# Kernel optimization log

Measured on AMD Instinct MI355X. Metric: run time of the kernel, lower is better.

The kernel has to match this reference:

```python
import jax, jax.numpy as jnp
import numpy as np

B, N, C = 4, 2048, 1024
H = 16
HD = C // H
SCALE = HD ** -0.5


def setup_inputs() -> dict:
    key = jax.random.key(0)
    ks = jax.random.split(key, 5)
    s = 0.02
    return {
        "x": jax.random.normal(ks[0], (B, N, C), dtype=jnp.float32),
        "w_qkv": jax.random.normal(ks[1], (C, 3 * C), dtype=jnp.float32) * s,
        "b_qkv": jnp.zeros((3 * C,), dtype=jnp.float32),
        "w_proj": jax.random.normal(ks[2], (C, C), dtype=jnp.float32) * s,
        "b_proj": jnp.zeros((C,), dtype=jnp.float32),
    }


def reference(x, w_qkv, b_qkv, w_proj, b_proj):
    b, n, c = x.shape
    qkv = x @ w_qkv + b_qkv                       # [b, n, 3c]
    qkv = qkv.reshape(b, n, 3, H, HD)
    qkv = jnp.transpose(qkv, (2, 0, 3, 1, 4))     # [3, b, h, n, hd]
    q, k, v = qkv[0], qkv[1], qkv[2]
    attn = jnp.einsum("bhqd,bhkd->bhqk", q, k) * SCALE
    attn = jax.nn.softmax(attn, axis=-1)
    out = jnp.einsum("bhqk,bhkd->bhqd", attn, v)  # [b, h, n, hd]
    out = jnp.transpose(out, (0, 2, 1, 3)).reshape(b, n, c)
    return out @ w_proj + b_proj
```

## Files before the change

### kernel.cpp

```cpp
#include <hip/hip_runtime.h>
#include <cstdint>
#include <cstddef>


typedef __attribute__((ext_vector_type(8))) short short8;
typedef __attribute__((ext_vector_type(4))) float f32x4;
typedef _Float16 half4 __attribute__((ext_vector_type(4)));

#if __has_builtin(__builtin_amdgcn_exp2f)
#define EXP2F(x) __builtin_amdgcn_exp2f(x)
#else
#define EXP2F(x) __expf((x) * 0.69314718056f)
#endif

__device__ __forceinline__ short f2bf(float x) {
  unsigned u = __builtin_bit_cast(unsigned, x);
  u += 0x7fffu + ((u >> 16) & 1u);
  return (short)(u >> 16);
}

__device__ __forceinline__ unsigned pkh(float a, float b) {
  auto h = __builtin_amdgcn_cvt_pkrtz(a, b);
  return __builtin_bit_cast(unsigned, h);
}

__device__ __forceinline__ void async16(const void* g, void* l) {
  __builtin_amdgcn_global_load_lds(
      (const __attribute__((address_space(1))) unsigned*)g,
      (__attribute__((address_space(3))) unsigned*)l, 16, 0, 0);
}


__global__ __launch_bounds__(256) void convert_kernel(const float* __restrict__ in,
                                                      short* __restrict__ out) {
  int i = blockIdx.x * 256 + threadIdx.x;
  const float4* p = (const float4*)in + (size_t)i * 2;
  float4 a = p[0], b = p[1];
  short8 r;
  r[0] = f2bf(a.x); r[1] = f2bf(a.y); r[2] = f2bf(a.z); r[3] = f2bf(a.w);
  r[4] = f2bf(b.x); r[5] = f2bf(b.y); r[6] = f2bf(b.z); r[7] = f2bf(b.w);
  *((short8*)out + i) = r;
}

__global__ __launch_bounds__(256) void wtrans_kernel(const float* __restrict__ in,
                                                     short* __restrict__ out,
                                                     int K, int N) {
  __shared__ float tile[32][33];
  int n0 = blockIdx.x * 32, k0 = blockIdx.y * 32;
  int tx = threadIdx.x, ty = threadIdx.y;
  for (int r = ty; r < 32; r += 8)
    tile[r][tx] = in[(size_t)(k0 + r) * N + n0 + tx];
  __syncthreads();
  for (int r = ty; r < 32; r += 8)
    out[(size_t)(n0 + r) * K + k0 + tx] = f2bf(tile[tx][r]);
}


template <int MODE>
__global__ __launch_bounds__(512, 2) void gemm_kernel(
    const short* __restrict__ A, const short* __restrict__ Bt,
    const float* __restrict__ bias, int Nn,
    short* __restrict__ qb, short* __restrict__ kb, short* __restrict__ vtb,
    float* __restrict__ outp) {
  constexpr int K = 1024;
  constexpr int NT = K / 64;
  __shared__ __align__(16) short As[3][256 * 64];
  __shared__ __align__(16) short Bs[3][128 * 64];
  const int tid = threadIdx.x, wave = tid >> 6, lane = tid & 63;
  const int quad = lane >> 4, l16 = lane & 15;

  const unsigned bid = blockIdx.x + gridDim.x * blockIdx.y;
  const unsigned c = bid & 7u, j = bid >> 3;
  const unsigned MC = gridDim.y >> 3;
  const unsigned chunk = MC * 8u;
  const unsigned nc = j / chunk, rem = j - nc * chunk;
  const unsigned m_idx = c * MC + (rem >> 3);
  const unsigned n_idx = nc * 8u + (rem & 7u);
  const int m0 = (int)m_idx * 256, n0 = (int)n_idx * 128;

  const int wrow = (wave >> 1) * 64, wcol = (wave & 1) * 64;

  const int srow = tid >> 3;
  const int schunk = ((tid & 7) ^ (srow & 7)) * 8;
  const short* Ag = A + (size_t)(m0 + srow) * K + schunk;
  const short* Bg = Bt + (size_t)(n0 + srow) * K + schunk;
  const int fsw = l16 & 7;

  f32x4 acc[4][4] = {};
  short8 af[4][2], bf[2][2];

  auto stageA = [&](int b, int kt) {
#pragma unroll
    for (int i = 0; i < 4; ++i)
      async16(Ag + (size_t)(i * 64) * K + kt * 64,
              (char*)As[b] + i * 8192 + tid * 16);
  };
  auto stageB = [&](int b, int kt) {
#pragma unroll
    for (int i = 0; i < 2; ++i)
      async16(Bg + (size_t)(i * 64) * K + kt * 64,
              (char*)Bs[b] + i * 8192 + tid * 16);
  };

  stageA(0, 0); stageB(0, 0);
  stageA(1, 1); stageB(1, 1);
  asm volatile("s_waitcnt vmcnt(6)" ::: "memory");
  __builtin_amdgcn_s_barrier();

  int cb = 0;
  for (int t = 0; t < NT; ++t) {
    int sb = cb + 2; if (sb >= 3) sb -= 3;
    const short* Ab = As[cb];
    const short* Bb = Bs[cb];

#pragma unroll
    for (int mf = 0; mf < 4; ++mf)
#pragma unroll
      for (int ks = 0; ks < 2; ++ks)
        af[mf][ks] = *(const short8*)
            &Ab[(wrow + mf * 16 + l16) * 64 + (((ks * 4 + quad) ^ fsw) << 3)];
#pragma unroll
    for (int j2 = 0; j2 < 2; ++j2)
#pragma unroll
      for (int ks = 0; ks < 2; ++ks)
        bf[j2][ks] = *(const short8*)
            &Bb[(wcol + j2 * 16 + l16) * 64 + (((ks * 4 + quad) ^ fsw) << 3)];
    if (t + 2 < NT) stageA(sb, t + 2);
    __builtin_amdgcn_s_barrier();
    __builtin_amdgcn_s_setprio(1);
#pragma unroll
    for (int ks = 0; ks < 2; ++ks)
#pragma unroll
      for (int mf = 0; mf < 4; ++mf)
#pragma unroll
        for (int j2 = 0; j2 < 2; ++j2)
          acc[mf][j2] = __builtin_amdgcn_mfma_f32_16x16x32_bf16(
              af[mf][ks], bf[j2][ks], acc[mf][j2], 0, 0, 0);
    __builtin_amdgcn_s_setprio(0);
    __builtin_amdgcn_s_barrier();

#pragma unroll
    for (int j2 = 0; j2 < 2; ++j2)
#pragma unroll
      for (int ks = 0; ks < 2; ++ks)
        bf[j2][ks] = *(const short8*)
            &Bb[(wcol + (2 + j2) * 16 + l16) * 64 + (((ks * 4 + quad) ^ fsw) << 3)];
    if (t + 2 < NT) stageB(sb, t + 2);
    __builtin_amdgcn_s_barrier();
    __builtin_amdgcn_s_setprio(1);
#pragma unroll
    for (int ks = 0; ks < 2; ++ks)
#pragma unroll
      for (int mf = 0; mf < 4; ++mf)
#pragma unroll
        for (int j2 = 0; j2 < 2; ++j2)
          acc[mf][2 + j2] = __builtin_amdgcn_mfma_f32_16x16x32_bf16(
              af[mf][ks], bf[j2][ks], acc[mf][2 + j2], 0, 0, 0);
    __builtin_amdgcn_s_setprio(0);
    if (t < NT - 2)
      asm volatile("s_waitcnt vmcnt(6)" ::: "memory");
    else if (t == NT - 2)
      asm volatile("s_waitcnt vmcnt(0)" ::: "memory");
    __builtin_amdgcn_s_barrier();
    cb = cb + 1; if (cb >= 3) cb -= 3;
  }

  if (MODE == 0) {
#pragma unroll
    for (int mf = 0; mf < 4; ++mf) {
      int row0 = m0 + wrow + mf * 16 + quad * 4;
      int b = row0 >> 11, n = row0 & 2047;
#pragma unroll
      for (int nf = 0; nf < 4; ++nf) {
        int col = n0 + wcol + nf * 16 + l16;
        float bv = bias[col];
        float v0 = acc[mf][nf][0] + bv, v1 = acc[mf][nf][1] + bv;
        float v2 = acc[mf][nf][2] + bv, v3 = acc[mf][nf][3] + bv;
        int which = col >> 10;
        int h = (col >> 6) & 15;
        int d = col & 63;
        size_t bh = (size_t)(b * 16 + h);
        if (which == 0) {
          const float qs = 0.18033688f;
          size_t base = (bh * 2048 + n) * 64 + d;
          qb[base]       = f2bf(v0 * qs);
          qb[base + 64]  = f2bf(v1 * qs);
          qb[base + 128] = f2bf(v2 * qs);
          qb[base + 192] = f2bf(v3 * qs);
        } else if (which == 1) {
          size_t base = (bh * 2048 + n) * 64 + d;
          kb[base]       = f2bf(v0);
          kb[base + 64]  = f2bf(v1);
          kb[base + 128] = f2bf(v2);
          kb[base + 192] = f2bf(v3);
        } else {
          uint2 pk;
          pk.x = pkh(v0, v1);
          pk.y = pkh(v2, v3);
          *(uint2*)&vtb[(bh * 64 + d) * 2048 + n] = pk;
        }
      }
    }
  } else {
#pragma unroll
    for (int mf = 0; mf < 4; ++mf) {
      int row0 = m0 + wrow + mf * 16 + quad * 4;
#pragma unroll
      for (int nf = 0; nf < 4; ++nf) {
        int col = n0 + wcol + nf * 16 + l16;
        float bv = bias[col];
        outp[(size_t)row0 * Nn + col]       = acc[mf][nf][0] + bv;
        outp[(size_t)(row0 + 1) * Nn + col] = acc[mf][nf][1] + bv;
        outp[(size_t)(row0 + 2) * Nn + col] = acc[mf][nf][2] + bv;
        outp[(size_t)(row0 + 3) * Nn + col] = acc[mf][nf][3] + bv;
      }
    }
  }
}


__global__ __launch_bounds__(256, 4) void attn_kernel(
    const short* __restrict__ qb, const short* __restrict__ kb,
    const short* __restrict__ vtb, short* __restrict__ ob) {
  __shared__ __align__(16) short Ks[2][64 * 64];
  __shared__ __align__(16) short Vs[2][64 * 64];
  __shared__ __align__(16) float Ls[4][32];
  const int tid = threadIdx.x, wave = tid >> 6, lane = tid & 63;
  const int quad = lane >> 4, l16 = lane & 15;
  int nlin = blockIdx.x + blockIdx.y * 16;
  nlin = (nlin & 7) * 128 + (nlin >> 3);
  const int q0 = (nlin & 15) * 128;
  const int bh = nlin >> 4;
  const short* Qg = qb + (size_t)bh * (2048 * 64);
  const short* Kg = kb + (size_t)bh * (2048 * 64);
  const short* Vg = vtb + (size_t)bh * (64 * 2048);

  short8 qf[2][2];
#pragma unroll
  for (int qt = 0; qt < 2; ++qt)
#pragma unroll
    for (int kc = 0; kc < 2; ++kc)
      qf[qt][kc] = *(const short8*)
          &Qg[(size_t)(q0 + wave * 32 + qt * 16 + l16) * 64 + kc * 32 + quad * 8];

  const int str = lane >> 3;
  const int sgc = ((lane & 7) ^ (str & 7)) * 8;
  const int fsw = l16 & 7;
  const int c0 = wave * 2, c1 = wave * 2 + 1;

  async16(Kg + (size_t)(c0 * 8 + str) * 64 + sgc, (char*)Ks[0] + c0 * 1024);
  async16(Kg + (size_t)(c1 * 8 + str) * 64 + sgc, (char*)Ks[0] + c1 * 1024);
  async16(Vg + (size_t)(c0 * 8 + str) * 2048 + sgc, (char*)Vs[0] + c0 * 1024);
  async16(Vg + (size_t)(c1 * 8 + str) * 2048 + sgc, (char*)Vs[0] + c1 * 1024);

  float lsum[2] = {0.f, 0.f};
  f32x4 oacc[2][4] = {};

  for (int t = 0; t < 32; ++t) {
    __syncthreads();

    int kvn = (t + 1) * 64;
    if (kvn < 2048) {
      char* kd = (char*)Ks[(t + 1) & 1];
      char* vd = (char*)Vs[(t + 1) & 1];
      async16(Kg + (size_t)(kvn + c0 * 8 + str) * 64 + sgc, kd + c0 * 1024);
      async16(Kg + (size_t)(kvn + c1 * 8 + str) * 64 + sgc, kd + c1 * 1024);
      async16(Vg + (size_t)(c0 * 8 + str) * 2048 + kvn + sgc, vd + c0 * 1024);
      async16(Vg + (size_t)(c1 * 8 + str) * 2048 + kvn + sgc, vd + c1 * 1024);
    }
    const short* Kst = Ks[t & 1];
    const short* Vst = Vs[t & 1];

    f32x4 sacc[2][4] = {};
#pragma unroll
    for (int kc = 0; kc < 2; ++kc) {
      short8 kf[4];
#pragma unroll
      for (int kvt = 0; kvt < 4; ++kvt)
        kf[kvt] = *(const short8*)
            &Kst[(kvt * 16 + l16) * 64 + (((kc * 4 + quad) ^ fsw) << 3)];
#pragma unroll
      for (int kvt = 0; kvt < 4; ++kvt)
#pragma unroll
        for (int qt = 0; qt < 2; ++qt)
          sacc[qt][kvt] = __builtin_amdgcn_mfma_f32_16x16x32_bf16(
              kf[kvt], qf[qt][kc], sacc[qt][kvt], 0, 0, 0);
    }

#pragma unroll
    for (int kvt = 0; kvt < 4; ++kvt) {
      half4 pfr[2];
#pragma unroll
      for (int qt = 0; qt < 2; ++qt) {
        float p0 = EXP2F(sacc[qt][kvt][0]);
        float p1 = EXP2F(sacc[qt][kvt][1]);
        float p2 = EXP2F(sacc[qt][kvt][2]);
        float p3 = EXP2F(sacc[qt][kvt][3]);
        lsum[qt] += (p0 + p1) + (p2 + p3);
        uint2 w;
        w.x = pkh(p0, p1);
        w.y = pkh(p2, p3);
        pfr[qt] = __builtin_bit_cast(half4, w);
      }
      const int vcol = (((kvt * 2 + (quad >> 1)) ^ fsw) << 3) + (quad & 1) * 4;
#pragma unroll
      for (int nt = 0; nt < 4; ++nt) {
        uint2 vr = *(const uint2*)&Vst[(nt * 16 + l16) * 64 + vcol];
        half4 vfr = __builtin_bit_cast(half4, vr);
#pragma unroll
        for (int qt = 0; qt < 2; ++qt)
          oacc[qt][nt] = __builtin_amdgcn_mfma_f32_16x16x16f16(
              pfr[qt], vfr, oacc[qt][nt], 0, 0, 0);
      }
    }
  }

#pragma unroll
  for (int qt = 0; qt < 2; ++qt) {
    float v = lsum[qt];
    v += __shfl_xor(v, 16, 64);
    v += __shfl_xor(v, 32, 64);
    if (quad == 0) Ls[wave][qt * 16 + l16] = v;
  }
  __asm__ volatile("s_waitcnt lgkmcnt(0)" ::: "memory");
  __builtin_amdgcn_wave_barrier();

  const int b = bh >> 4, h = bh & 15;
#pragma unroll
  for (int qt = 0; qt < 2; ++qt) {
    float4 lr = *(const float4*)&Ls[wave][qt * 16 + quad * 4];
    float inv0 = 1.f / lr.x, inv1 = 1.f / lr.y, inv2 = 1.f / lr.z, inv3 = 1.f / lr.w;
#pragma unroll
    for (int nt = 0; nt < 4; ++nt) {
      int d = nt * 16 + l16;
      int qbase = q0 + wave * 32 + qt * 16 + quad * 4;
      size_t obase = ((size_t)(b * 2048 + qbase)) * 1024 + h * 64 + d;
      ob[obase]        = f2bf(oacc[qt][nt][0] * inv0);
      ob[obase + 1024] = f2bf(oacc[qt][nt][1] * inv1);
      ob[obase + 2048] = f2bf(oacc[qt][nt][2] * inv2);
      ob[obase + 3072] = f2bf(oacc[qt][nt][3] * inv3);
    }
  }
}


extern "C" void kernel_launch(void* const* d_in, const int* in_sizes, int n_in,
                              void* d_out, int out_size, void* d_ws, size_t ws_size,
                              hipStream_t stream) {
  const float* x      = (const float*)d_in[0];
  const float* w_qkv  = (const float*)d_in[1];
  const float* b_qkv  = (const float*)d_in[2];
  const float* w_proj = (const float*)d_in[3];
  const float* b_proj = (const float*)d_in[4];
  float* out = (float*)d_out;

  short* xs     = (short*)d_ws;
  short* wqkvT  = xs + (size_t)8192 * 1024;
  short* wprojT = wqkvT + (size_t)3072 * 1024;
  short* qb     = wprojT + (size_t)1024 * 1024;
  short* kb     = qb + (size_t)64 * 2048 * 64;
  short* vtb    = kb + (size_t)64 * 2048 * 64;
  short* aob    = vtb + (size_t)64 * 2048 * 64;

  convert_kernel<<<dim3(4096), 256, 0, stream>>>(x, xs);
  wtrans_kernel<<<dim3(96, 32), dim3(32, 8), 0, stream>>>(w_qkv, wqkvT, 1024, 3072);
  wtrans_kernel<<<dim3(32, 32), dim3(32, 8), 0, stream>>>(w_proj, wprojT, 1024, 1024);

  gemm_kernel<0><<<dim3(24, 32), 512, 0, stream>>>(xs, wqkvT, b_qkv, 3072,
                                                   qb, kb, vtb, nullptr);
  attn_kernel<<<dim3(16, 64), 256, 0, stream>>>(qb, kb, vtb, aob);
  gemm_kernel<1><<<dim3(8, 32), 512, 0, stream>>>(aob, wprojT, b_proj, 1024,
                                                  nullptr, nullptr, nullptr, out);
}
```

Measured before the change: 278.1 us.

## Use 16x16x32 f16 MFMA for PV via cross-lane P fragment permutes

Replaces the PV product's 16x16x16 f16 MFMAs with 16x16x32 f16 MFMAs, which halves the MFMA instruction count and uses 16-byte V fragment loads from LDS. The QK^T and softmax step is split into two 32-key blocks. P fragments are rearranged across lanes with ds_bpermute so that 8 contiguous keys land in each lane. This adds eight bpermute LDS operations and selects per block, which may compete with the V reads for LDS bandwidth.

Result: slower. 291.9 us (+5.0%).

```diff
diff --git a/kernel.cpp b/kernel.cpp
--- a/kernel.cpp
+++ b/kernel.cpp
@@ -6,6 +6,7 @@
 typedef __attribute__((ext_vector_type(8))) short short8;
 typedef __attribute__((ext_vector_type(4))) float f32x4;
 typedef _Float16 half4 __attribute__((ext_vector_type(4)));
+typedef _Float16 half8 __attribute__((ext_vector_type(8)));
 
 #if __has_builtin(__builtin_amdgcn_exp2f)
 #define EXP2F(x) __builtin_amdgcn_exp2f(x)
@@ -248,6 +249,10 @@
   const int fsw = l16 & 7;
   const int c0 = wave * 2, c1 = wave * 2 + 1;
 
+  const int adA = ((lane & 16) ? 128 : 0) + l16 * 4;
+  const int adB = adA + 64;
+  const bool hiq = (lane & 32) != 0;
+
   async16(Kg + (size_t)(c0 * 8 + str) * 64 + sgc, (char*)Ks[0] + c0 * 1024);
   async16(Kg + (size_t)(c1 * 8 + str) * 64 + sgc, (char*)Ks[0] + c1 * 1024);
   async16(Vg + (size_t)(c0 * 8 + str) * 2048 + sgc, (char*)Vs[0] + c0 * 1024);
@@ -271,46 +276,65 @@
     const short* Kst = Ks[t & 1];
     const short* Vst = Vs[t & 1];
 
-    f32x4 sacc[2][4] = {};
-#pragma unroll
-    for (int kc = 0; kc < 2; ++kc) {
-      short8 kf[4];
-#pragma unroll
-      for (int kvt = 0; kvt < 4; ++kvt)
-        kf[kvt] = *(const short8*)
-            &Kst[(kvt * 16 + l16) * 64 + (((kc * 4 + quad) ^ fsw) << 3)];
-#pragma unroll
-      for (int kvt = 0; kvt < 4; ++kvt)
+#pragma unroll
+    for (int blk = 0; blk < 2; ++blk) {
+      f32x4 sacc[2][2] = {};
+#pragma unroll
+      for (int kc = 0; kc < 2; ++kc) {
+        short8 kf[2];
+#pragma unroll
+        for (int vv = 0; vv < 2; ++vv)
+          kf[vv] = *(const short8*)
+              &Kst[((blk * 2 + vv) * 16 + l16) * 64 + (((kc * 4 + quad) ^ fsw) << 3)];
+#pragma unroll
+        for (int vv = 0; vv < 2; ++vv)
+#pragma unroll
+          for (int qt = 0; qt < 2; ++qt)
+            sacc[qt][vv] = __builtin_amdgcn_mfma_f32_16x16x32_bf16(
+                kf[vv], qf[qt][kc], sacc[qt][vv], 0, 0, 0);
+      }
+
+      unsigned pk[2][2][2];
+#pragma unroll
+      for (int qt = 0; qt < 2; ++qt)
+#pragma unroll
+        for (int vv = 0; vv < 2; ++vv) {
+          float p0 = EXP2F(sacc[qt][vv][0]);
+          float p1 = EXP2F(sacc[qt][vv][1]);
+          float p2 = EXP2F(sacc[qt][vv][2]);
+          float p3 = EXP2F(sacc[qt][vv][3]);
+          lsum[qt] += (p0 + p1) + (p2 + p3);
+          pk[qt][vv][0] = pkh(p0, p1);
+          pk[qt][vv][1] = pkh(p2, p3);
+        }
+
+      half8 pf[2];
+#pragma unroll
+      for (int qt = 0; qt < 2; ++qt) {
+        int e0 = __builtin_amdgcn_ds_bpermute(adA, (int)pk[qt][0][0]);
+        int o0 = __builtin_amdgcn_ds_bpermute(adA, (int)pk[qt][1][0]);
+        int e1 = __builtin_amdgcn_ds_bpermute(adA, (int)pk[qt][0][1]);
+        int o1 = __builtin_amdgcn_ds_bpermute(adA, (int)pk[qt][1][1]);
+        int e2 = __builtin_amdgcn_ds_bpermute(adB, (int)pk[qt][0][0]);
+        int o2 = __builtin_amdgcn_ds_bpermute(adB, (int)pk[qt][1][0]);
+        int e3 = __builtin_amdgcn_ds_bpermute(adB, (int)pk[qt][0][1]);
+        int o3 = __builtin_amdgcn_ds_bpermute(adB, (int)pk[qt][1][1]);
+        uint4 wv;
+        wv.x = (unsigned)(hiq ? o0 : e0);
+        wv.y = (unsigned)(hiq ? o1 : e1);
+        wv.z = (unsigned)(hiq ? o2 : e2);
+        wv.w = (unsigned)(hiq ? o3 : e3);
+        pf[qt] = __builtin_bit_cast(half8, wv);
+      }
+
+#pragma unroll
+      for (int nt = 0; nt < 4; ++nt) {
+        half8 vf = *(const half8*)
+            &Vst[(nt * 16 + l16) * 64 + (((blk * 4 + quad) ^ fsw) << 3)];
 #pragma unroll
         for (int qt = 0; qt < 2; ++qt)
-          sacc[qt][kvt] = __builtin_amdgcn_mfma_f32_16x16x32_bf16(
-              kf[kvt], qf[qt][kc], sacc[qt][kvt], 0, 0, 0);
-    }
-
-#pragma unroll
-    for (int kvt = 0; kvt < 4; ++kvt) {
-      half4 pfr[2];
-#pragma unroll
-      for (int qt = 0; qt < 2; ++qt) {
-        float p0 = EXP2F(sacc[qt][kvt][0]);
-        float p1 = EXP2F(sacc[qt][kvt][1]);
-        float p2 = EXP2F(sacc[qt][kvt][2]);
-        float p3 = EXP2F(sacc[qt][kvt][3]);
-        lsum[qt] += (p0 + p1) + (p2 + p3);
-        uint2 w;
-        w.x = pkh(p0, p1);
-        w.y = pkh(p2, p3);
-        pfr[qt] = __builtin_bit_cast(half4, w);
-      }
-      const int vcol = (((kvt * 2 + (quad >> 1)) ^ fsw) << 3) + (quad & 1) * 4;
-#pragma unroll
-      for (int nt = 0; nt < 4; ++nt) {
-        uint2 vr = *(const uint2*)&Vst[(nt * 16 + l16) * 64 + vcol];
-        half4 vfr = __builtin_bit_cast(half4, vr);
-#pragma unroll
-        for (int qt = 0; qt < 2; ++qt)
-          oacc[qt][nt] = __builtin_amdgcn_mfma_f32_16x16x16f16(
-              pfr[qt], vfr, oacc[qt][nt], 0, 0, 0);
+          oacc[qt][nt] = __builtin_amdgcn_mfma_f32_16x16x32_f16(
+              pf[qt], vf, oacc[qt][nt], 0, 0, 0);
       }
     }
   }
```
